# Performance work log

Measured on AMD Instinct MI355X. Metric: run time of the kernel, lower is better.

Reference implementation:

```python
import jax, jax.numpy as jnp
import numpy as np

B, N, HID = 2, 2048, 1024
NH = 16
HD = HID // NH

def setup_inputs() -> dict:
    key = jax.random.key(0)
    ks = jax.random.split(key, 5)
    s = 0.02
    return {
        "hidden_states": jax.random.normal(ks[0], (B, N, HID), jnp.float32),
        "attention_mask": jnp.zeros((B, 1, 1, N), jnp.float32),
        "Wq": jax.random.normal(ks[1], (HID, HID), jnp.float32) * s,
        "bq": jnp.zeros((HID,), jnp.float32),
        "Wk": jax.random.normal(ks[2], (HID, HID), jnp.float32) * s,
        "bk": jnp.zeros((HID,), jnp.float32),
        "Wv": jax.random.normal(ks[3], (HID, HID), jnp.float32) * s,
        "bv": jnp.zeros((HID,), jnp.float32),
    }

def reference(hidden_states, attention_mask, Wq, bq, Wk, bk, Wv, bv):
    b, n, _ = hidden_states.shape
    def split_heads(t):  # [b,n,hid] -> [b,h,n,d]
        return t.reshape(b, n, NH, HD).transpose(0, 2, 1, 3)
    q = split_heads(hidden_states @ Wq.T + bq)
    k = split_heads(hidden_states @ Wk.T + bk)
    v = split_heads(hidden_states @ Wv.T + bv)
    scores = jnp.einsum('bhnd,bhmd->bhnm', q, k) / jnp.sqrt(jnp.float32(HD)).astype(q.dtype)
    scores = scores + attention_mask
    scores = jnp.maximum(scores, jnp.finfo(scores.dtype).min)
    probs = jax.nn.softmax(scores, axis=-1)
    out = jnp.einsum('bhnm,bhmd->bhnd', probs, v)
    return out.transpose(0, 2, 1, 3).reshape(b, n, NH * HD)
```

## Files before the change

### kernel.cpp

```cpp
#include <hip/hip_runtime.h>

typedef unsigned short u16;
typedef unsigned int   u32;
typedef __attribute__((ext_vector_type(8))) short bf16x8;
typedef __attribute__((ext_vector_type(4))) float f32x4;
typedef __attribute__((ext_vector_type(2))) unsigned int u32x2;

__device__ __forceinline__ float bf2f(u16 u) { return __uint_as_float(((u32)u) << 16); }
__device__ __forceinline__ u16 f2bf(float f) {
    return (u16)((__float_as_uint(f) + 0x8000u) >> 16);
}
__device__ __forceinline__ u32 cvt_pk_bf16(float lo, float hi) {
    u32 r;
    asm("v_cvt_pk_bf16_f32 %0, %1, %2" : "=v"(r) : "v"(lo), "v"(hi));
    return r;
}
__device__ __forceinline__ void gload16(const void* g, void* l) {
    __builtin_amdgcn_global_load_lds((const __attribute__((address_space(1))) void*)g,
                                     (__attribute__((address_space(3))) void*)l, 16, 0, 0);
}
#define VMCNT(n) asm volatile("s_waitcnt vmcnt(" #n ")" ::: "memory")

struct us4 { u16 x, y, z, w; };
__global__ void cvt_all(const float* __restrict__ hs, const float* __restrict__ wq,
                        const float* __restrict__ wk, const float* __restrict__ wv,
                        u16* __restrict__ dst)
{
    int i = blockIdx.x * blockDim.x + threadIdx.x;
    const int stride = gridDim.x * blockDim.x;
    us4* d4 = (us4*)dst;
    for (; i < 1835008; i += stride) {
        const float4* s4;
        int j = i;
        if (j < 1048576)      { s4 = (const float4*)hs; }
        else if (j < 1310720) { s4 = (const float4*)wq; j -= 1048576; }
        else if (j < 1572864) { s4 = (const float4*)wk; j -= 1310720; }
        else                  { s4 = (const float4*)wv; j -= 1572864; }
        float4 v = s4[j];
        us4 o;
        o.x = f2bf(v.x); o.y = f2bf(v.y); o.z = f2bf(v.z); o.w = f2bf(v.w);
        d4[i] = o;
    }
}

__global__ __launch_bounds__(256) void qkv_gemm(
    const u16* __restrict__ hs,
    const u16* __restrict__ Wq, const u16* __restrict__ Wk, const u16* __restrict__ Wv,
    const float* __restrict__ bq, const float* __restrict__ bk, const float* __restrict__ bv,
    u16* __restrict__ oq, u16* __restrict__ ok, u16* __restrict__ ovt)
{
    __shared__ u16 smem[32768];
    u16* sA0 = smem;
    u16* sB0 = smem + 8192;
    u16* sA1 = smem + 16384;
    u16* sB1 = smem + 24576;

    const int tid  = threadIdx.x;
    const int lane = tid & 63;
    const int w    = tid >> 6;
    const int c15  = lane & 15;
    const int q4   = lane >> 4;
    const int mat  = blockIdx.x >> 3;
    const int cb   = blockIdx.x & 7;
    const int rb   = blockIdx.y;
    const int wr   = w >> 1, wc = w & 1;

    const u16*   W    = (mat == 0) ? Wq : (mat == 1 ? Wk : Wv);
    const float* bias = (mat == 0) ? bq : (mat == 1 ? bk : bv);

    f32x4 acc[4][4] = {};

    const int rs = tid >> 3;
    const int cs = ((tid & 7) ^ (rs & 7)) * 8;
    const u16* gA = hs + (rb * 128) * 1024;
    const u16* gB = W + (cb * 128) * 1024;

    auto stageQ = [&](u16* dA, u16* dB, int kb) {
#pragma unroll
        for (int p = 0; p < 4; ++p)
            gload16(gA + (rs + 32 * p) * 1024 + kb + cs, dA + p * 2048 + w * 512);
#pragma unroll
        for (int p = 0; p < 4; ++p)
            gload16(gB + (rs + 32 * p) * 1024 + kb + cs, dB + p * 2048 + w * 512);
    };

    auto computeQ = [&](const u16* sA, const u16* sB) {
        __builtin_amdgcn_s_setprio(1);
#pragma unroll
        for (int kk = 0; kk < 2; ++kk) {
            const int cpos = ((kk * 4 + q4) ^ (c15 & 7)) * 8;
            bf16x8 af[4], bf[4];
#pragma unroll
            for (int mt = 0; mt < 4; ++mt)
                af[mt] = *(const bf16x8*)(sA + (wr * 64 + mt * 16 + c15) * 64 + cpos);
#pragma unroll
            for (int nt = 0; nt < 4; ++nt)
                bf[nt] = *(const bf16x8*)(sB + (wc * 64 + nt * 16 + c15) * 64 + cpos);
#pragma unroll
            for (int mt = 0; mt < 4; ++mt)
#pragma unroll
                for (int nt = 0; nt < 4; ++nt)
                    acc[mt][nt] = __builtin_amdgcn_mfma_f32_16x16x32_bf16(
                        af[mt], bf[nt], acc[mt][nt], 0, 0, 0);
        }
        __builtin_amdgcn_s_setprio(0);
    };

    stageQ(sA0, sB0, 0);
    stageQ(sA1, sB1, 64);

#pragma unroll 1
    for (int T = 0; T < 14; T += 2) {
        VMCNT(8);
        __builtin_amdgcn_s_barrier();
        __builtin_amdgcn_sched_barrier(0);
        computeQ(sA0, sB0);
        __builtin_amdgcn_s_barrier();
        __builtin_amdgcn_sched_barrier(0);
        stageQ(sA0, sB0, (T + 2) * 64);

        VMCNT(8);
        __builtin_amdgcn_s_barrier();
        __builtin_amdgcn_sched_barrier(0);
        computeQ(sA1, sB1);
        __builtin_amdgcn_s_barrier();
        __builtin_amdgcn_sched_barrier(0);
        stageQ(sA1, sB1, (T + 3) * 64);
    }
    VMCNT(8);
    __builtin_amdgcn_s_barrier();
    __builtin_amdgcn_sched_barrier(0);
    computeQ(sA0, sB0);
    VMCNT(0);
    __builtin_amdgcn_s_barrier();
    __builtin_amdgcn_sched_barrier(0);
    computeQ(sA1, sB1);

    __syncthreads();
    const int h = cb * 2 + wc;
    float bvv[4];
#pragma unroll
    for (int nt = 0; nt < 4; ++nt)
        bvv[nt] = bias[cb * 128 + wc * 64 + nt * 16 + c15];

    u16* sc = smem + w * 4608;
    if (mat != 2) {
        u16* dst = (mat == 0) ? oq : ok;
#pragma unroll
        for (int mt = 0; mt < 4; ++mt)
#pragma unroll
            for (int nt = 0; nt < 4; ++nt)
#pragma unroll
                for (int rr = 0; rr < 4; ++rr)
                    sc[(mt * 16 + q4 * 4 + rr) * 72 + nt * 16 + c15] =
                        f2bf(acc[mt][nt][rr] + bvv[nt]);
#pragma unroll
        for (int p = 0; p < 8; ++p) {
            const int s = p * 64 + lane;
            const int rl = s >> 3, oct = (s & 7) * 8;
            bf16x8 vv = *(const bf16x8*)(sc + rl * 72 + oct);
            const int n = rb * 128 + wr * 64 + rl;
            const int bb = n >> 11, nn = n & 2047;
            *(bf16x8*)(dst + (((bb * 16 + h) * 2048) + nn) * 64 + oct) = vv;
        }
    } else {
#pragma unroll
        for (int mt = 0; mt < 4; ++mt)
#pragma unroll
            for (int nt = 0; nt < 4; ++nt)
#pragma unroll
                for (int rr = 0; rr < 4; ++rr)
                    sc[(nt * 16 + c15) * 72 + mt * 16 + q4 * 4 + rr] =
                        f2bf(acc[mt][nt][rr] + bvv[nt]);
#pragma unroll
        for (int p = 0; p < 8; ++p) {
            const int s = p * 64 + lane;
            const int dr = s >> 3, noct = (s & 7) * 8;
            bf16x8 vv = *(const bf16x8*)(sc + dr * 72 + noct);
            const int n0 = rb * 128 + wr * 64 + noct;
            const int bb = n0 >> 11, nn = n0 & 2047;
            *(bf16x8*)(ovt + ((bb * 16 + h) * 64 + dr) * 2048 + nn) = vv;
        }
    }
}

__global__ __launch_bounds__(256, 4) void attn(
    const u16* __restrict__ qm, const u16* __restrict__ km, const u16* __restrict__ vtm,
    const float* __restrict__ mask, float* __restrict__ out)
{
    __shared__ u16 sK0[4096];
    __shared__ u16 sV0[4096];
    __shared__ u16 sK1[4096];
    __shared__ u16 sV1[4096];

    const int tid = threadIdx.x, lane = tid & 63, w = tid >> 6;
    const int c15 = lane & 15, q4 = lane >> 4;
    const int bh = blockIdx.x;
    const int qt = blockIdx.y;
    const int b = bh >> 4;

    bf16x8 qf[2];
    const u16* qbase = qm + (bh * 2048 + qt * 64 + w * 16) * 64;
#pragma unroll
    for (int kt = 0; kt < 2; ++kt)
        qf[kt] = *(const bf16x8*)(qbase + c15 * 64 + kt * 32 + q4 * 8);

    float l_acc = 0.f;
    f32x4 accO[4] = {};

    const u16* kbase  = km  + bh * 2048 * 64;
    const u16* vtbase = vtm + bh * 64 * 2048;

    const int rs   = tid >> 3;
    const int cls  = ((tid & 7) ^ (rs & 7)) * 8;
    const int prK  = (rs & 3) | ((rs & 0x0C) << 1) | ((rs & 0x10) >> 2);
    const int ldsW = w * 512;

    const float* mbase = mask + b * 2048 + 8 * q4;

    auto stage = [&](u16* dK, u16* dV, int TT) {
        const u16* kg = kbase + TT * 64 * 64;
        const u16* vg = vtbase + TT * 64;
#pragma unroll
        for (int p = 0; p < 2; ++p)
            gload16(kg + (prK + 32 * p) * 64 + cls, dK + p * 2048 + ldsW);
#pragma unroll
        for (int p = 0; p < 2; ++p)
            gload16(vg + (rs + 32 * p) * 2048 + cls, dV + p * 2048 + ldsW);
    };

    auto compute64 = [&](const u16* sKh, const u16* sVT, int kb) {
        float mkv[4][4];
#pragma unroll
        for (int t = 0; t < 4; ++t) {
            float4 m4 = *(const float4*)(mbase + kb + 32 * (t >> 1) + 4 * (t & 1));
            mkv[t][0] = m4.x * 1.4426950408889634f;
            mkv[t][1] = m4.y * 1.4426950408889634f;
            mkv[t][2] = m4.z * 1.4426950408889634f;
            mkv[t][3] = m4.w * 1.4426950408889634f;
        }

        f32x4 accST[4] = {};
        __builtin_amdgcn_s_setprio(1);
#pragma unroll
        for (int kt = 0; kt < 2; ++kt) {
            bf16x8 kf[4];
#pragma unroll
            for (int t = 0; t < 4; ++t) {
                const int rho = t * 16 + c15;
                const int cpos = (kt * 4 + q4) ^ (rho & 7);
                kf[t] = *(const bf16x8*)(sKh + rho * 64 + cpos * 8);
            }
#pragma unroll
            for (int t = 0; t < 4; ++t)
                accST[t] = __builtin_amdgcn_mfma_f32_16x16x32_bf16(
                    kf[t], qf[kt], accST[t], 0, 0, 0);
        }
        __builtin_amdgcn_s_setprio(0);

        u32 pu[4][2];
#pragma unroll
        for (int t = 0; t < 4; ++t) {
            float p[4];
#pragma unroll
            for (int rr = 0; rr < 4; ++rr)
                p[rr] = __builtin_amdgcn_exp2f(
                    fmaf(accST[t][rr], 0.18033688011112042f, mkv[t][rr]));
            l_acc += (p[0] + p[1]) + (p[2] + p[3]);
            pu[t][0] = cvt_pk_bf16(p[0], p[1]);
            pu[t][1] = cvt_pk_bf16(p[2], p[3]);
        }

        __builtin_amdgcn_s_setprio(1);
#pragma unroll
        for (int g = 0; g < 2; ++g) {
            bf16x8 vB[4];
#pragma unroll
            for (int nt = 0; nt < 4; ++nt) {
                const int d = nt * 16 + c15;
                const int pc = (4 * g + q4) ^ (d & 7);
                vB[nt] = *(const bf16x8*)(sVT + d * 64 + pc * 8);
            }
            union { bf16x8 v; u32 u[4]; } ta;
            ta.u[0] = pu[2 * g][0];
            ta.u[1] = pu[2 * g][1];
            ta.u[2] = pu[2 * g + 1][0];
            ta.u[3] = pu[2 * g + 1][1];
#pragma unroll
            for (int nt = 0; nt < 4; ++nt)
                accO[nt] = __builtin_amdgcn_mfma_f32_16x16x32_bf16(
                    ta.v, vB[nt], accO[nt], 0, 0, 0);
        }
        __builtin_amdgcn_s_setprio(0);
    };

    stage(sK0, sV0, 0);
    stage(sK1, sV1, 1);

#pragma unroll 1
    for (int T = 0; T < 30; T += 2) {
        VMCNT(4);
        __builtin_amdgcn_s_barrier();
        __builtin_amdgcn_sched_barrier(0);
        compute64(sK0, sV0, T * 64);
        __builtin_amdgcn_s_barrier();
        __builtin_amdgcn_sched_barrier(0);
        stage(sK0, sV0, T + 2);

        VMCNT(4);
        __builtin_amdgcn_s_barrier();
        __builtin_amdgcn_sched_barrier(0);
        compute64(sK1, sV1, (T + 1) * 64);
        __builtin_amdgcn_s_barrier();
        __builtin_amdgcn_sched_barrier(0);
        stage(sK1, sV1, T + 3);
    }
    VMCNT(4);
    __builtin_amdgcn_s_barrier();
    __builtin_amdgcn_sched_barrier(0);
    compute64(sK0, sV0, 30 * 64);
    VMCNT(0);
    __builtin_amdgcn_s_barrier();
    __builtin_amdgcn_sched_barrier(0);
    compute64(sK1, sV1, 31 * 64);

    l_acc += __shfl_xor(l_acc, 16);
    l_acc += __shfl_xor(l_acc, 32);

    const int h = bh & 15;
    float inv[4];
#pragma unroll
    for (int rr = 0; rr < 4; ++rr)
        inv[rr] = 1.0f / __shfl(l_acc, q4 * 4 + rr);
#pragma unroll
    for (int nt = 0; nt < 4; ++nt)
#pragma unroll
        for (int rr = 0; rr < 4; ++rr) {
            const int qrow = qt * 64 + w * 16 + q4 * 4 + rr;
            const int d = nt * 16 + c15;
            out[(b * 2048 + qrow) * 1024 + h * 64 + d] = accO[nt][rr] * inv[rr];
        }
}

extern "C" void kernel_launch(void* const* d_in, const int* in_sizes, int n_in,
                              void* d_out, int out_size, void* d_ws, size_t ws_size,
                              hipStream_t stream)
{
    const float* hs   = (const float*)d_in[0];
    const float* mask = (const float*)d_in[1];
    const float* Wq   = (const float*)d_in[2];
    const float* bq   = (const float*)d_in[3];
    const float* Wk   = (const float*)d_in[4];
    const float* bk   = (const float*)d_in[5];
    const float* Wv   = (const float*)d_in[6];
    const float* bv   = (const float*)d_in[7];

    u16* ws   = (u16*)d_ws;
    u16* qw   = ws;
    u16* kw   = ws + 4194304;
    u16* vtw  = ws + 8388608;
    u16* hsb  = ws + 12582912;
    u16* wqb  = ws + 16777216;
    u16* wkb  = ws + 17825792;
    u16* wvb  = ws + 18874368;

    cvt_all<<<1024, 256, 0, stream>>>(hs, Wq, Wk, Wv, hsb);

    qkv_gemm<<<dim3(24, 32), 256, 0, stream>>>(hsb, wqb, wkb, wvb, bq, bk, bv, qw, kw, vtw);
    attn<<<dim3(32, 32), 256, 0, stream>>>(qw, kw, vtw, mask, (float*)d_out);
}
```

Baseline: 167.1 us.

## Split attention keys across waves with register-direct K/V loads and LDS reduction

```diff
diff --git a/kernel.cpp b/kernel.cpp
--- a/kernel.cpp
+++ b/kernel.cpp
@@ -4,7 +4,6 @@
 typedef unsigned int   u32;
 typedef __attribute__((ext_vector_type(8))) short bf16x8;
 typedef __attribute__((ext_vector_type(4))) float f32x4;
-typedef __attribute__((ext_vector_type(2))) unsigned int u32x2;
 
 __device__ __forceinline__ float bf2f(u16 u) { return __uint_as_float(((u32)u) << 16); }
 __device__ __forceinline__ u16 f2bf(float f) {
@@ -184,161 +183,180 @@
     }
 }
 
-__global__ __launch_bounds__(256, 4) void attn(
+__global__ __launch_bounds__(256, 2) void attn(
     const u16* __restrict__ qm, const u16* __restrict__ km, const u16* __restrict__ vtm,
     const float* __restrict__ mask, float* __restrict__ out)
 {
-    __shared__ u16 sK0[4096];
-    __shared__ u16 sV0[4096];
-    __shared__ u16 sK1[4096];
-    __shared__ u16 sV1[4096];
+    __shared__ float obuf[8192];
+    __shared__ float lbuf[4][4][16];
 
     const int tid = threadIdx.x, lane = tid & 63, w = tid >> 6;
     const int c15 = lane & 15, q4 = lane >> 4;
     const int bh = blockIdx.x;
     const int qt = blockIdx.y;
-    const int b = bh >> 4;
-
-    bf16x8 qf[2];
-    const u16* qbase = qm + (bh * 2048 + qt * 64 + w * 16) * 64;
-#pragma unroll
-    for (int kt = 0; kt < 2; ++kt)
-        qf[kt] = *(const bf16x8*)(qbase + c15 * 64 + kt * 32 + q4 * 8);
-
-    float l_acc = 0.f;
-    f32x4 accO[4] = {};
-
-    const u16* kbase  = km  + bh * 2048 * 64;
-    const u16* vtbase = vtm + bh * 64 * 2048;
-
-    const int rs   = tid >> 3;
-    const int cls  = ((tid & 7) ^ (rs & 7)) * 8;
-    const int prK  = (rs & 3) | ((rs & 0x0C) << 1) | ((rs & 0x10) >> 2);
-    const int ldsW = w * 512;
-
-    const float* mbase = mask + b * 2048 + 8 * q4;
-
-    auto stage = [&](u16* dK, u16* dV, int TT) {
-        const u16* kg = kbase + TT * 64 * 64;
-        const u16* vg = vtbase + TT * 64;
-#pragma unroll
-        for (int p = 0; p < 2; ++p)
-            gload16(kg + (prK + 32 * p) * 64 + cls, dK + p * 2048 + ldsW);
-#pragma unroll
-        for (int p = 0; p < 2; ++p)
-            gload16(vg + (rs + 32 * p) * 2048 + cls, dV + p * 2048 + ldsW);
+    const int b = bh >> 4, h = bh & 15;
+
+    bf16x8 qf[4][2];
+    const u16* qbase = qm + (bh * 2048 + qt * 64) * 64;
+#pragma unroll
+    for (int qt4 = 0; qt4 < 4; ++qt4)
+#pragma unroll
+        for (int kt = 0; kt < 2; ++kt)
+            qf[qt4][kt] = *(const bf16x8*)(qbase + (qt4 * 16 + c15) * 64 + kt * 32 + q4 * 8);
+
+    const int vb16 = ((c15 >> 2) << 3) | (c15 & 3);
+    const u16* kb_ = km + (bh * 2048 + w * 32 + vb16) * 64 + q4 * 8;
+    const u16* vb_ = vtm + bh * 64 * 2048 + c15 * 2048 + w * 32 + q4 * 8;
+    const float* mb_ = mask + b * 2048 + w * 32 + q4 * 8;
+
+    float l_part[4] = {0.f, 0.f, 0.f, 0.f};
+    f32x4 accO[4][4] = {};
+
+    auto loadPair = [&](bf16x8 (&kf)[2][2], bf16x8 (&vv)[4], float4 (&mm)[2], int it) {
+        const int ko = it * 8192;
+        const int vo = it * 128;
+#pragma unroll
+        for (int kap = 0; kap < 2; ++kap)
+#pragma unroll
+            for (int kt = 0; kt < 2; ++kt)
+                kf[kap][kt] = *(const bf16x8*)(kb_ + ko + kap * 256 + kt * 32);
+#pragma unroll
+        for (int nt = 0; nt < 4; ++nt)
+            vv[nt] = *(const bf16x8*)(vb_ + nt * 32768 + vo);
+#pragma unroll
+        for (int kap = 0; kap < 2; ++kap)
+            mm[kap] = *(const float4*)(mb_ + vo + kap * 4);
     };
 
-    auto compute64 = [&](const u16* sKh, const u16* sVT, int kb) {
-        float mkv[4][4];
-#pragma unroll
-        for (int t = 0; t < 4; ++t) {
-            float4 m4 = *(const float4*)(mbase + kb + 32 * (t >> 1) + 4 * (t & 1));
-            mkv[t][0] = m4.x * 1.4426950408889634f;
-            mkv[t][1] = m4.y * 1.4426950408889634f;
-            mkv[t][2] = m4.z * 1.4426950408889634f;
-            mkv[t][3] = m4.w * 1.4426950408889634f;
-        }
-
-        f32x4 accST[4] = {};
+    auto computePair = [&](const bf16x8 (&kf)[2][2], const bf16x8 (&vv)[4],
+                           const float4 (&mm)[2]) {
+        f32x4 accST[2][4] = {};
         __builtin_amdgcn_s_setprio(1);
 #pragma unroll
-        for (int kt = 0; kt < 2; ++kt) {
-            bf16x8 kf[4];
-#pragma unroll
-            for (int t = 0; t < 4; ++t) {
-                const int rho = t * 16 + c15;
-                const int cpos = (kt * 4 + q4) ^ (rho & 7);
-                kf[t] = *(const bf16x8*)(sKh + rho * 64 + cpos * 8);
+        for (int kap = 0; kap < 2; ++kap)
+#pragma unroll
+            for (int kt = 0; kt < 2; ++kt)
+#pragma unroll
+                for (int qt4 = 0; qt4 < 4; ++qt4)
+                    accST[kap][qt4] = __builtin_amdgcn_mfma_f32_16x16x32_bf16(
+                        kf[kap][kt], qf[qt4][kt], accST[kap][qt4], 0, 0, 0);
+        __builtin_amdgcn_s_setprio(0);
+
+        u32 pu[2][4][2];
+#pragma unroll
+        for (int kap = 0; kap < 2; ++kap) {
+            const float m0 = mm[kap].x * 1.4426950408889634f;
+            const float m1 = mm[kap].y * 1.4426950408889634f;
+            const float m2 = mm[kap].z * 1.4426950408889634f;
+            const float m3 = mm[kap].w * 1.4426950408889634f;
+#pragma unroll
+            for (int qt4 = 0; qt4 < 4; ++qt4) {
+                const float p0 = __builtin_amdgcn_exp2f(
+                    fmaf(accST[kap][qt4][0], 0.18033688011112042f, m0));
+                const float p1 = __builtin_amdgcn_exp2f(
+                    fmaf(accST[kap][qt4][1], 0.18033688011112042f, m1));
+                const float p2 = __builtin_amdgcn_exp2f(
+                    fmaf(accST[kap][qt4][2], 0.18033688011112042f, m2));
+                const float p3 = __builtin_amdgcn_exp2f(
+                    fmaf(accST[kap][qt4][3], 0.18033688011112042f, m3));
+                l_part[qt4] += (p0 + p1) + (p2 + p3);
+                pu[kap][qt4][0] = cvt_pk_bf16(p0, p1);
+                pu[kap][qt4][1] = cvt_pk_bf16(p2, p3);
             }
-#pragma unroll
-            for (int t = 0; t < 4; ++t)
-                accST[t] = __builtin_amdgcn_mfma_f32_16x16x32_bf16(
-                    kf[t], qf[kt], accST[t], 0, 0, 0);
-        }
-        __builtin_amdgcn_s_setprio(0);
-
-        u32 pu[4][2];
-#pragma unroll
-        for (int t = 0; t < 4; ++t) {
-            float p[4];
-#pragma unroll
-            for (int rr = 0; rr < 4; ++rr)
-                p[rr] = __builtin_amdgcn_exp2f(
-                    fmaf(accST[t][rr], 0.18033688011112042f, mkv[t][rr]));
-            l_acc += (p[0] + p[1]) + (p[2] + p[3]);
-            pu[t][0] = cvt_pk_bf16(p[0], p[1]);
-            pu[t][1] = cvt_pk_bf16(p[2], p[3]);
         }
 
         __builtin_amdgcn_s_setprio(1);
 #pragma unroll
-        for (int g = 0; g < 2; ++g) {
-            bf16x8 vB[4];
-#pragma unroll
-            for (int nt = 0; nt < 4; ++nt) {
-                const int d = nt * 16 + c15;
-                const int pc = (4 * g + q4) ^ (d & 7);
-                vB[nt] = *(const bf16x8*)(sVT + d * 64 + pc * 8);
-            }
+        for (int qt4 = 0; qt4 < 4; ++qt4) {
             union { bf16x8 v; u32 u[4]; } ta;
-            ta.u[0] = pu[2 * g][0];
-            ta.u[1] = pu[2 * g][1];
-            ta.u[2] = pu[2 * g + 1][0];
-            ta.u[3] = pu[2 * g + 1][1];
-#pragma unroll
-            for (int nt = 0; nt < 4; ++nt)
-                accO[nt] = __builtin_amdgcn_mfma_f32_16x16x32_bf16(
-                    ta.v, vB[nt], accO[nt], 0, 0, 0);
+            ta.u[0] = pu[0][qt4][0];
+            ta.u[1] = pu[0][qt4][1];
+            ta.u[2] = pu[1][qt4][0];
+            ta.u[3] = pu[1][qt4][1];
+#pragma unroll
+            for (int nt = 0; nt < 4; ++nt)
+                accO[qt4][nt] = __builtin_amdgcn_mfma_f32_16x16x32_bf16(
+                    vv[nt], ta.v, accO[qt4][nt], 0, 0, 0);
         }
         __builtin_amdgcn_s_setprio(0);
     };
 
-    stage(sK0, sV0, 0);
-    stage(sK1, sV1, 1);
+    bf16x8 kA[2][2], kB[2][2], vA[4], vB[4];
+    float4 mA[2], mB[2];
+    loadPair(kA, vA, mA, 0);
+    loadPair(kB, vB, mB, 1);
 
 #pragma unroll 1
-    for (int T = 0; T < 30; T += 2) {
-        VMCNT(4);
-        __builtin_amdgcn_s_barrier();
-        __builtin_amdgcn_sched_barrier(0);
-        compute64(sK0, sV0, T * 64);
-        __builtin_amdgcn_s_barrier();
-        __builtin_amdgcn_sched_barrier(0);
-        stage(sK0, sV0, T + 2);
-
-        VMCNT(4);
-        __builtin_amdgcn_s_barrier();
-        __builtin_amdgcn_sched_barrier(0);
-        compute64(sK1, sV1, (T + 1) * 64);
-        __builtin_amdgcn_s_barrier();
-        __builtin_amdgcn_sched_barrier(0);
-        stage(sK1, sV1, T + 3);
-    }
-    VMCNT(4);
-    __builtin_amdgcn_s_barrier();
-    __builtin_amdgcn_sched_barrier(0);
-    compute64(sK0, sV0, 30 * 64);
-    VMCNT(0);
-    __builtin_amdgcn_s_barrier();
-    __builtin_amdgcn_sched_barrier(0);
-    compute64(sK1, sV1, 31 * 64);
-
-    l_acc += __shfl_xor(l_acc, 16);
-    l_acc += __shfl_xor(l_acc, 32);
-
-    const int h = bh & 15;
-    float inv[4];
-#pragma unroll
-    for (int rr = 0; rr < 4; ++rr)
-        inv[rr] = 1.0f / __shfl(l_acc, q4 * 4 + rr);
-#pragma unroll
-    for (int nt = 0; nt < 4; ++nt)
-#pragma unroll
-        for (int rr = 0; rr < 4; ++rr) {
-            const int qrow = qt * 64 + w * 16 + q4 * 4 + rr;
-            const int d = nt * 16 + c15;
-            out[(b * 2048 + qrow) * 1024 + h * 64 + d] = accO[nt][rr] * inv[rr];
+    for (int T = 0; T < 14; T += 2) {
+        computePair(kA, vA, mA);
+        loadPair(kA, vA, mA, T + 2);
+        computePair(kB, vB, mB);
+        loadPair(kB, vB, mB, T + 3);
+    }
+    computePair(kA, vA, mA);
+    computePair(kB, vB, mB);
+
+#pragma unroll
+    for (int qt4 = 0; qt4 < 4; ++qt4) {
+        l_part[qt4] += __shfl_xor(l_part[qt4], 16);
+        l_part[qt4] += __shfl_xor(l_part[qt4], 32);
+    }
+    if (q4 == 0)
+#pragma unroll
+        for (int qt4 = 0; qt4 < 4; ++qt4)
+            lbuf[w][qt4][c15] = l_part[qt4];
+
+    const int mh = w >> 1;
+    const int p1 = w ^ 2, p2 = w ^ 1;
+#pragma unroll
+    for (int qt4 = 0; qt4 < 4; ++qt4)
+        if ((qt4 >> 1) != mh) {
+            const int rel = qt4 & 1;
+#pragma unroll
+            for (int nt = 0; nt < 4; ++nt)
+                *(float4*)&obuf[w * 2048 + (rel * 4 + nt) * 256 + lane * 4] =
+                    *(const float4*)&accO[qt4][nt];
+        }
+    __syncthreads();
+#pragma unroll
+    for (int qt4 = 0; qt4 < 4; ++qt4)
+        if ((qt4 >> 1) == mh) {
+            const int rel = qt4 & 1;
+#pragma unroll
+            for (int nt = 0; nt < 4; ++nt) {
+                float4 v4 = *(const float4*)&obuf[p1 * 2048 + (rel * 4 + nt) * 256 + lane * 4];
+                accO[qt4][nt][0] += v4.x; accO[qt4][nt][1] += v4.y;
+                accO[qt4][nt][2] += v4.z; accO[qt4][nt][3] += v4.w;
+            }
+        }
+    __syncthreads();
+#pragma unroll
+    for (int qt4 = 0; qt4 < 4; ++qt4)
+        if (qt4 == p2)
+#pragma unroll
+            for (int nt = 0; nt < 4; ++nt)
+                *(float4*)&obuf[w * 2048 + nt * 256 + lane * 4] =
+                    *(const float4*)&accO[qt4][nt];
+    __syncthreads();
+
+#pragma unroll
+    for (int qt4 = 0; qt4 < 4; ++qt4)
+        if (qt4 == w) {
+            const float lt = lbuf[0][qt4][c15] + lbuf[1][qt4][c15] +
+                             lbuf[2][qt4][c15] + lbuf[3][qt4][c15];
+            const float inv = 1.0f / lt;
+            const int qrow = qt * 64 + qt4 * 16 + c15;
+            float* ob = out + (b * 2048 + qrow) * 1024 + h * 64 + q4 * 4;
+#pragma unroll
+            for (int nt = 0; nt < 4; ++nt) {
+                float4 v4 = *(const float4*)&obuf[p2 * 2048 + nt * 256 + lane * 4];
+                float4 o;
+                o.x = (accO[qt4][nt][0] + v4.x) * inv;
+                o.y = (accO[qt4][nt][1] + v4.y) * inv;
+                o.z = (accO[qt4][nt][2] + v4.z) * inv;
+                o.w = (accO[qt4][nt][3] + v4.w) * inv;
+                *(float4*)(ob + nt * 16) = o;
+            }
         }
 }
 
```

After: 188.7 us. 1.13x slower.
